# Optimization experiments

Measured on AMD Instinct MI355X. Metric: run time of the kernel, lower is better.

## Reference

```python
import jax, jax.numpy as jnp
import numpy as np

ALPHA = 0.2  # LeakyReLU negative slope

def setup_inputs() -> dict:
    key = jax.random.key(0)
    k1, k2, k3 = jax.random.split(key, 3)
    B, N, Fin, Fout = 8, 2048, 256, 128
    h = jax.random.normal(k1, (B, N, Fin), dtype=jnp.float32)
    W = jax.random.normal(k2, (Fin, Fout), dtype=jnp.float32) * (1.414 / np.sqrt(Fin))
    a = jax.random.normal(k3, (2 * Fout, 1), dtype=jnp.float32) * 0.1
    return {"h": h, "W": W, "a": a}

def reference(h, W, a):
    # Wh: [B, N, D]
    Wh = jnp.einsum('bni,io->bno', h, W)
    D = Wh.shape[-1]
    a1 = a[:D, 0]   # weights for the 'i' (repeat_interleave) half
    a2 = a[D:, 0]   # weights for the 'j' (repeat) half
    s1 = Wh @ a1    # [B, N]
    s2 = Wh @ a2    # [B, N]
    # e[b,i,j] = leakyrelu(s1[b,i] + s2[b,j])  (fused form of the O(N^2*2D) concat)
    e = s1[:, :, None] + s2[:, None, :]
    e = jnp.where(e >= 0, e, ALPHA * e)
    # original applies softmax over dim=1 (the i axis)
    attention = jax.nn.softmax(e, axis=1)
    # dropout is identity in eval mode
    h_prime = jnp.einsum('bij,bjd->bid', attention, Wh)
    # concat=True -> ELU
    return jax.nn.elu(h_prime)
```

## Files before the change

kernel.cpp:

```cpp
#include <hip/hip_runtime.h>
#include <hip/hip_bf16.h>


#define ALPHA 0.2f
#define LOG2E 1.4426950408889634f
constexpr int Bb=8, Nn=2048, FIN=256, FOUT=128;

typedef __attribute__((ext_vector_type(8))) short short8;
typedef __attribute__((ext_vector_type(4))) float f32x4;
typedef __attribute__((ext_vector_type(16))) float f32x16;
typedef const __attribute__((address_space(1))) unsigned int* gptr_t;
typedef __attribute__((address_space(3))) unsigned int* lptr_t;

__device__ __forceinline__ float lrelu(float x){ return fmaxf(x, ALPHA*x); }
__device__ __forceinline__ unsigned short bfbits(float x){
    __hip_bfloat16 h = __float2bfloat16(x);
    return *(unsigned short*)&h;
}

__global__ __launch_bounds__(256) void k_wh(const float* __restrict__ h,
                                            const float* __restrict__ W,
                                            const float* __restrict__ a,
                                            float* __restrict__ s1,
                                            float* __restrict__ s2,
                                            __hip_bfloat16* __restrict__ WhT){
    const int blk = blockIdx.x;
    const int rowbase = blk * 32;
    const int b = blk >> 6;
    const int jt = (rowbase & (Nn-1)) >> 5;
    const int t = threadIdx.x;
    const int wave = t>>6, lane = t&63;
    const int wm = wave & 1, wn = wave >> 1;
    const int lm = lane & 15, q = lane >> 4;

    __shared__ __align__(16) float hs[32*260];
    __shared__ float s1red[2][32], s2red[2][32];

    {
        const float* srcbase = h + (size_t)rowbase*FIN;
        #pragma unroll
        for (int c = 0; c < 8; ++c){
            const int row = wave*8 + c;
            __builtin_amdgcn_global_load_lds(
                (gptr_t)(srcbase + (size_t)row*FIN + lane*4),
                (lptr_t)&hs[row*260], 16, 0, 0);
        }
    }
    __syncthreads();

    f32x4 acc[4];
    #pragma unroll
    for (int ntl = 0; ntl < 4; ++ntl) acc[ntl] = (f32x4){0.f,0.f,0.f,0.f};

    const float* hrow = &hs[(wm*16 + lm)*260];
    const float* Wq   = W + (size_t)(q*8)*FOUT + wn*64 + lm;
    #pragma unroll
    for (int kt = 0; kt < 8; ++kt){
        float av[8];
        *(float4*)&av[0] = *(const float4*)&hrow[kt*32 + q*8];
        *(float4*)&av[4] = *(const float4*)&hrow[kt*32 + q*8 + 4];
        short8 afr;
        #pragma unroll
        for (int e = 0; e < 8; ++e) afr[e] = (short)bfbits(av[e]);
        const float* Wkt = Wq + (size_t)kt*32*FOUT;
        #pragma unroll
        for (int ntl = 0; ntl < 4; ++ntl){
            const float* Wp = Wkt + ntl*16;
            short8 bfr;
            #pragma unroll
            for (int e = 0; e < 8; ++e) bfr[e] = (short)bfbits(Wp[(size_t)e*FOUT]);
            acc[ntl] = __builtin_amdgcn_mfma_f32_16x16x32_bf16(afr, bfr, acc[ntl], 0,0,0);
        }
    }

    {
        float a1v[4], a2v[4];
        #pragma unroll
        for (int ntl = 0; ntl < 4; ++ntl){
            a1v[ntl] = a[wn*64 + ntl*16 + lm];
            a2v[ntl] = a[FOUT + wn*64 + ntl*16 + lm];
        }
        #pragma unroll
        for (int rg = 0; rg < 4; ++rg){
            float p1 = 0.f, p2 = 0.f;
            #pragma unroll
            for (int ntl = 0; ntl < 4; ++ntl){
                p1 += acc[ntl][rg]*a1v[ntl];
                p2 += acc[ntl][rg]*a2v[ntl];
            }
            #pragma unroll
            for (int m = 1; m < 16; m <<= 1){
                p1 += __shfl_xor(p1, m);
                p2 += __shfl_xor(p2, m);
            }
            if (lm == 0){
                s1red[wn][wm*16 + q*4 + rg] = p1;
                s2red[wn][wm*16 + q*4 + rg] = p2;
            }
        }
    }

    {
        short* Wo = (short*)WhT;
        const size_t tb = ((size_t)(b*32 + (jt >> 1)))*8192;
        const int s  = (jt & 1)*2 + wm;
        const int l5 = q >> 1, ehalf = (q & 1)*4;
        #pragma unroll
        for (int ntl = 0; ntl < 4; ++ntl){
            const int d = wn*64 + ntl*16 + lm;
            const int u = (s*4 + (d>>5))*64 + l5*32 + (d & 31);
            ushort4 v;
            v.x = bfbits(acc[ntl][0]); v.y = bfbits(acc[ntl][1]);
            v.z = bfbits(acc[ntl][2]); v.w = bfbits(acc[ntl][3]);
            *(ushort4*)&Wo[tb + (size_t)u*8 + ehalf] = v;
        }
    }

    __syncthreads();
    if (t < 32){
        s1[rowbase + t] = (s1red[0][t] + s1red[1][t]) * LOG2E;
        s2[rowbase + t] = (s2red[0][t] + s2red[1][t]) * LOG2E;
    }
}

__global__ __launch_bounds__(256) void k_z(const float* __restrict__ s1,
                                           const float* __restrict__ s2,
                                           float* __restrict__ Aout,
                                           float* __restrict__ Bout){
    const int b  = blockIdx.x >> 6;
    const int jt = blockIdx.x & 63;
    const int t  = threadIdx.x;
    const int jj = t & 31, part = t >> 5;
    const int j  = jt*32 + jj;
    __shared__ float s1s[Nn];
    __shared__ float red[8][33];

    {
        const float4* g = (const float4*)(s1 + (size_t)b*Nn);
        float4* p = (float4*)s1s;
        #pragma unroll
        for (int v0 = 0; v0 < 2; ++v0){ const int v = t + v0*256; p[v] = g[v]; }
    }
    __syncthreads();
    const float s2j = s2[b*Nn + j];
    float sum = 0.f;
    const float4* s4 = (const float4*)&s1s[part*256];
    #pragma unroll 4
    for (int v = 0; v < 64; ++v){
        float x[4]; *(float4*)x = s4[v];
        sum += __builtin_amdgcn_exp2f(lrelu(x[0]+s2j))
             + __builtin_amdgcn_exp2f(lrelu(x[1]+s2j))
             + __builtin_amdgcn_exp2f(lrelu(x[2]+s2j))
             + __builtin_amdgcn_exp2f(lrelu(x[3]+s2j));
    }
    red[part][jj] = sum;
    __syncthreads();
    if (part == 0){
        float Z = 0.f;
        #pragma unroll
        for (int p = 0; p < 8; ++p) Z += red[p][jj];
        const float lz = -__builtin_amdgcn_logf(Z);
        Aout[b*Nn + j] = s2j + lz;
        Bout[b*Nn + j] = ALPHA*s2j + lz;
    }
}

__global__ __launch_bounds__(512, 2) void k_pv(const float* __restrict__ s1,
                                               const float* __restrict__ Aarr,
                                               const float* __restrict__ Barr,
                                               const __hip_bfloat16* __restrict__ WhT,
                                               float* __restrict__ out){
    const int blk   = blockIdx.x;
    const int b     = blk & 7;
    const int ibase = (blk >> 3) * 64;
    const int t     = threadIdx.x;
    const int wave  = t >> 6, lane = t & 63;
    const int wr = wave & 1, kh = wave >> 1;
    const int il = lane & 31, l5 = lane >> 5;

    __shared__ unsigned short Bs[2][4][8192];

    const float s1a  = s1[(size_t)b*Nn + ibase + wr*32 + il];
    const float as1a = ALPHA * s1a;
    const float* Ab = Aarr + (size_t)b*Nn;
    const float* Zb = Barr + (size_t)b*Nn;

    f32x16 acc[4];
    #pragma unroll
    for (int nt = 0; nt < 4; ++nt)
        #pragma unroll
        for (int e = 0; e < 16; ++e) acc[nt][e] = 0.f;

    const char* Wtb = (const char*)WhT + (size_t)b*32*16384;
    const int laneoff = wr*8192 + lane*16;

    {
        const char* src = Wtb + (size_t)(kh*8)*16384 + laneoff;
        unsigned short* dst = &Bs[0][kh][wr*4096];
        #pragma unroll
        for (int c = 0; c < 8; ++c)
            __builtin_amdgcn_global_load_lds((gptr_t)(src + c*1024),
                                             (lptr_t)(dst + c*512), 16, 0, 0);
    }

    int buf = 0;
    for (int it = 0; it < 8; ++it){
        __syncthreads();
        if (it + 1 < 8){
            const char* src = Wtb + (size_t)(kh*8 + it + 1)*16384 + laneoff;
            unsigned short* dst = &Bs[buf^1][kh][wr*4096];
            #pragma unroll
            for (int c = 0; c < 8; ++c)
                __builtin_amdgcn_global_load_lds((gptr_t)(src + c*1024),
                                                 (lptr_t)(dst + c*512), 16, 0, 0);
        }
        const char* tile = (const char*)&Bs[buf][kh][0];
        #pragma unroll
        for (int s = 0; s < 4; ++s){
            short8 bfr[4];
            #pragma unroll
            for (int nt = 0; nt < 4; ++nt)
                bfr[nt] = *(const short8*)(tile + ((s*4 + nt)*64 + lane)*16);

            const int jb = kh*512 + it*64 + s*16 + l5*8;
            float av[8], bv[8];
            *(float4*)&av[0] = *(const float4*)&Ab[jb];
            *(float4*)&av[4] = *(const float4*)&Ab[jb+4];
            *(float4*)&bv[0] = *(const float4*)&Zb[jb];
            *(float4*)&bv[4] = *(const float4*)&Zb[jb+4];
            short8 afa;
            #pragma unroll
            for (int e = 0; e < 8; ++e)
                afa[e] = (short)bfbits(__builtin_amdgcn_exp2f(
                             fmaxf(s1a + av[e], as1a + bv[e])));
            #pragma unroll
            for (int nt = 0; nt < 4; ++nt)
                acc[nt] = __builtin_amdgcn_mfma_f32_32x32x16_bf16(afa, bfr[nt], acc[nt], 0,0,0);
        }
        buf ^= 1;
    }

    __syncthreads();
    float* comb = (float*)&Bs[0][0][0];
    if (kh < 2){
        float* cb = comb + (size_t)(kh*2 + wr)*(32*132);
        #pragma unroll
        for (int nt = 0; nt < 4; ++nt)
            #pragma unroll
            for (int r = 0; r < 16; ++r){
                const int row = (r&3) + 8*(r>>2) + 4*l5;
                cb[row*132 + nt*32 + il] = acc[nt][r];
            }
    }
    __syncthreads();
    if (kh >= 2){
        float* cb = comb + (size_t)((kh-2)*2 + wr)*(32*132);
        #pragma unroll
        for (int nt = 0; nt < 4; ++nt)
            #pragma unroll
            for (int r = 0; r < 16; ++r){
                const int row = (r&3) + 8*(r>>2) + 4*l5;
                cb[row*132 + nt*32 + il] += acc[nt][r];
            }
    }
    __syncthreads();
    {
        const int rgrp = t >> 5, c4 = (t & 31)*4;
        #pragma unroll
        for (int rr = 0; rr < 4; ++rr){
            const int row = rgrp*4 + rr;
            const int wrr = row >> 5, rin = row & 31;
            const float* r0 = comb + (size_t)(wrr)*(32*132)       + rin*132 + c4;
            const float* r1 = comb + (size_t)(2 + wrr)*(32*132)   + rin*132 + c4;
            float4 v0 = *(const float4*)r0, v1 = *(const float4*)r1;
            float o[4];
            #pragma unroll
            for (int e = 0; e < 4; ++e){
                const float x = ((const float*)&v0)[e] + ((const float*)&v1)[e];
                o[e] = x > 0.f ? x : expm1f(x);
            }
            *(float4*)&out[((size_t)(b*Nn + ibase + row))*FOUT + c4] = *(float4*)o;
        }
    }
}

extern "C" void kernel_launch(void* const* d_in, const int* in_sizes, int n_in,
                              void* d_out, int out_size, void* d_ws, size_t ws_size,
                              hipStream_t stream) {
    (void)in_sizes; (void)n_in; (void)out_size; (void)ws_size;
    const float* h = (const float*)d_in[0];
    const float* W = (const float*)d_in[1];
    const float* a = (const float*)d_in[2];
    float* out = (float*)d_out;

    float* ws    = (float*)d_ws;
    float* s1    = ws;
    float* s2    = s1 + Bb*Nn;
    float* Aarr  = s2 + Bb*Nn;
    float* Barr  = Aarr + Bb*Nn;
    __hip_bfloat16* WhT = (__hip_bfloat16*)(Barr + Bb*Nn);

    k_wh  <<<dim3(Bb*Nn/32),  dim3(256), 0, stream>>>(h, W, a, s1, s2, WhT);
    k_z   <<<dim3(Bb*64),     dim3(256), 0, stream>>>(s1, s2, Aarr, Barr);
    k_pv  <<<dim3(Bb*Nn/64),  dim3(512), 0, stream>>>(s1, Aarr, Barr, WhT, out);
}
```

Before: 105.2 us.

## Replace dense attention matmul with sort-and-prefix-sum separable LeakyReLU formulation

Uses the fact that exp(lrelu(s1_i+s2_j)) splits into exp(s1)exp(s2) or exp(a*s1)exp(a*s2) depending on the sign of s1_i+s2_j. It sorts s1 and s2 per batch, computes softmax normalisers with prefix and suffix sums plus binary search, and computes the output through chunked prefix sums of weighted Wh rows. This turns the O(N^2·D) MFMA attention into roughly O(N log N + N·D) work. In exchange it adds a serial bitonic sort in only 16 blocks, several extra launches, scattered gathers, and possible precision loss from the exp2 of unnormalised scores.

```diff
diff --git a/kernel.cpp b/kernel.cpp
--- a/kernel.cpp
+++ b/kernel.cpp
@@ -5,35 +5,38 @@
 #define ALPHA 0.2f
 #define LOG2E 1.4426950408889634f
 constexpr int Bb=8, Nn=2048, FIN=256, FOUT=128;
+constexpr int NC=32, CH=64;
+constexpr int SUFSTR=2052;
 
 typedef __attribute__((ext_vector_type(8))) short short8;
 typedef __attribute__((ext_vector_type(4))) float f32x4;
-typedef __attribute__((ext_vector_type(16))) float f32x16;
 typedef const __attribute__((address_space(1))) unsigned int* gptr_t;
 typedef __attribute__((address_space(3))) unsigned int* lptr_t;
 
-__device__ __forceinline__ float lrelu(float x){ return fmaxf(x, ALPHA*x); }
 __device__ __forceinline__ unsigned short bfbits(float x){
     __hip_bfloat16 h = __float2bfloat16(x);
     return *(unsigned short*)&h;
 }
+__device__ __forceinline__ float bf2f(unsigned short u){
+    unsigned int w = ((unsigned int)u) << 16;
+    return *(float*)&w;
+}
 
 __global__ __launch_bounds__(256) void k_wh(const float* __restrict__ h,
                                             const float* __restrict__ W,
                                             const float* __restrict__ a,
-                                            float* __restrict__ s1,
-                                            float* __restrict__ s2,
-                                            __hip_bfloat16* __restrict__ WhT){
+                                            float* __restrict__ s1h,
+                                            float* __restrict__ s2h,
+                                            __hip_bfloat16* __restrict__ Whb){
     const int blk = blockIdx.x;
     const int rowbase = blk * 32;
-    const int b = blk >> 6;
-    const int jt = (rowbase & (Nn-1)) >> 5;
     const int t = threadIdx.x;
     const int wave = t>>6, lane = t&63;
     const int wm = wave & 1, wn = wave >> 1;
     const int lm = lane & 15, q = lane >> 4;
 
     __shared__ __align__(16) float hs[32*260];
+    __shared__ __align__(16) float tt2[32][132];
     __shared__ float s1red[2][32], s2red[2][32];
 
     {
@@ -100,186 +103,277 @@
         }
     }
 
-    {
-        short* Wo = (short*)WhT;
-        const size_t tb = ((size_t)(b*32 + (jt >> 1)))*8192;
-        const int s  = (jt & 1)*2 + wm;
-        const int l5 = q >> 1, ehalf = (q & 1)*4;
-        #pragma unroll
-        for (int ntl = 0; ntl < 4; ++ntl){
-            const int d = wn*64 + ntl*16 + lm;
-            const int u = (s*4 + (d>>5))*64 + l5*32 + (d & 31);
-            ushort4 v;
-            v.x = bfbits(acc[ntl][0]); v.y = bfbits(acc[ntl][1]);
-            v.z = bfbits(acc[ntl][2]); v.w = bfbits(acc[ntl][3]);
-            *(ushort4*)&Wo[tb + (size_t)u*8 + ehalf] = v;
-        }
-    }
-
-    __syncthreads();
+    #pragma unroll
+    for (int ntl = 0; ntl < 4; ++ntl)
+        #pragma unroll
+        for (int rg = 0; rg < 4; ++rg)
+            tt2[wm*16 + q*4 + rg][wn*64 + ntl*16 + lm] = acc[ntl][rg];
+    __syncthreads();
+
     if (t < 32){
-        s1[rowbase + t] = (s1red[0][t] + s1red[1][t]) * LOG2E;
-        s2[rowbase + t] = (s2red[0][t] + s2red[1][t]) * LOG2E;
-    }
-}
-
-__global__ __launch_bounds__(256) void k_z(const float* __restrict__ s1,
-                                           const float* __restrict__ s2,
-                                           float* __restrict__ Aout,
-                                           float* __restrict__ Bout){
-    const int b  = blockIdx.x >> 6;
-    const int jt = blockIdx.x & 63;
-    const int t  = threadIdx.x;
-    const int jj = t & 31, part = t >> 5;
-    const int j  = jt*32 + jj;
-    __shared__ float s1s[Nn];
-    __shared__ float red[8][33];
-
-    {
-        const float4* g = (const float4*)(s1 + (size_t)b*Nn);
-        float4* p = (float4*)s1s;
-        #pragma unroll
-        for (int v0 = 0; v0 < 2; ++v0){ const int v = t + v0*256; p[v] = g[v]; }
-    }
-    __syncthreads();
-    const float s2j = s2[b*Nn + j];
-    float sum = 0.f;
-    const float4* s4 = (const float4*)&s1s[part*256];
-    #pragma unroll 4
-    for (int v = 0; v < 64; ++v){
-        float x[4]; *(float4*)x = s4[v];
-        sum += __builtin_amdgcn_exp2f(lrelu(x[0]+s2j))
-             + __builtin_amdgcn_exp2f(lrelu(x[1]+s2j))
-             + __builtin_amdgcn_exp2f(lrelu(x[2]+s2j))
-             + __builtin_amdgcn_exp2f(lrelu(x[3]+s2j));
-    }
-    red[part][jj] = sum;
-    __syncthreads();
-    if (part == 0){
-        float Z = 0.f;
-        #pragma unroll
-        for (int p = 0; p < 8; ++p) Z += red[p][jj];
-        const float lz = -__builtin_amdgcn_logf(Z);
-        Aout[b*Nn + j] = s2j + lz;
-        Bout[b*Nn + j] = ALPHA*s2j + lz;
-    }
-}
-
-__global__ __launch_bounds__(512, 2) void k_pv(const float* __restrict__ s1,
-                                               const float* __restrict__ Aarr,
-                                               const float* __restrict__ Barr,
-                                               const __hip_bfloat16* __restrict__ WhT,
-                                               float* __restrict__ out){
-    const int blk   = blockIdx.x;
-    const int b     = blk & 7;
-    const int ibase = (blk >> 3) * 64;
-    const int t     = threadIdx.x;
-    const int wave  = t >> 6, lane = t & 63;
-    const int wr = wave & 1, kh = wave >> 1;
-    const int il = lane & 31, l5 = lane >> 5;
-
-    __shared__ unsigned short Bs[2][4][8192];
-
-    const float s1a  = s1[(size_t)b*Nn + ibase + wr*32 + il];
-    const float as1a = ALPHA * s1a;
-    const float* Ab = Aarr + (size_t)b*Nn;
-    const float* Zb = Barr + (size_t)b*Nn;
-
-    f32x16 acc[4];
+        s1h[rowbase + t] = (s1red[0][t] + s1red[1][t]) * LOG2E;
+        s2h[rowbase + t] = (s2red[0][t] + s2red[1][t]) * LOG2E;
+    }
+    {
+        const int row = t >> 3, seg = (t & 7) * 16;
+        const float* src = &tt2[row][seg];
+        short8 v0, v1;
+        #pragma unroll
+        for (int e = 0; e < 8; ++e){
+            v0[e] = (short)bfbits(src[e]);
+            v1[e] = (short)bfbits(src[e+8]);
+        }
+        short* dst = (short*)Whb + (size_t)(rowbase + row)*FOUT + seg;
+        *(short8*)dst       = v0;
+        *(short8*)(dst + 8) = v1;
+    }
+}
+
+__global__ __launch_bounds__(1024) void k_sort(const float* __restrict__ s1h,
+                                               const float* __restrict__ s2h,
+                                               float* __restrict__ s1s,
+                                               float* __restrict__ s2s,
+                                               int* __restrict__ ipr,
+                                               int* __restrict__ prm,
+                                               float* __restrict__ SufE,
+                                               float* __restrict__ PreA){
+    const int bb = blockIdx.x;
+    const bool isS1 = bb >= 8;
+    const int b = bb & 7;
+    const int t = threadIdx.x;
+    __shared__ __align__(16) float key[2048];
+    __shared__ __align__(16) int   pay[2048];
+    __shared__ __align__(16) float scb[2048];
+
+    const float* src = (isS1 ? s1h : s2h) + (size_t)b*Nn;
     #pragma unroll
-    for (int nt = 0; nt < 4; ++nt)
-        #pragma unroll
-        for (int e = 0; e < 16; ++e) acc[nt][e] = 0.f;
-
-    const char* Wtb = (const char*)WhT + (size_t)b*32*16384;
-    const int laneoff = wr*8192 + lane*16;
-
-    {
-        const char* src = Wtb + (size_t)(kh*8)*16384 + laneoff;
-        unsigned short* dst = &Bs[0][kh][wr*4096];
-        #pragma unroll
-        for (int c = 0; c < 8; ++c)
-            __builtin_amdgcn_global_load_lds((gptr_t)(src + c*1024),
-                                             (lptr_t)(dst + c*512), 16, 0, 0);
-    }
-
-    int buf = 0;
-    for (int it = 0; it < 8; ++it){
+    for (int v=0; v<2; ++v){ const int i=t+v*1024; key[i]=src[i]; pay[i]=i; }
+    __syncthreads();
+    for (int k=2; k<=2048; k<<=1){
+        for (int j=k>>1; j>0; j>>=1){
+            const int i = ((t & ~(j-1))<<1) | (t & (j-1));
+            const int l = i | j;
+            const bool up = (i & k)==0;
+            const float a0=key[i], a1=key[l];
+            const bool sw = up ? (a0>a1) : (a0<a1);
+            if (sw){
+                key[i]=a1; key[l]=a0;
+                const int p0=pay[i]; pay[i]=pay[l]; pay[l]=p0;
+            }
+            __syncthreads();
+        }
+    }
+    {
+        float* kdst = (isS1 ? s1s : s2s) + (size_t)b*Nn;
+        int*   pdst = (isS1 ? ipr : prm) + (size_t)b*Nn;
+        #pragma unroll
+        for (int v=0; v<2; ++v){ const int i=t+v*1024; kdst[i]=key[i]; pdst[i]=pay[i]; }
+    }
+    if (isS1){
         __syncthreads();
-        if (it + 1 < 8){
-            const char* src = Wtb + (size_t)(kh*8 + it + 1)*16384 + laneoff;
-            unsigned short* dst = &Bs[buf^1][kh][wr*4096];
+        float* bufB = (float*)pay;
+        float* bufC = scb;
+
+        #pragma unroll
+        for (int v=0; v<2; ++v){ const int i=t+v*1024; bufB[i]=__builtin_amdgcn_exp2f(ALPHA*key[i]); }
+        __syncthreads();
+        {
+            float *sp=bufB, *dp=bufC;
+            for (int off=1; off<2048; off<<=1){
+                #pragma unroll
+                for (int v=0; v<2; ++v){
+                    const int i=t+v*1024;
+                    float x = sp[i];
+                    if (i>=off) x += sp[i-off];
+                    dp[i]=x;
+                }
+                __syncthreads();
+                float* tmp=sp; sp=dp; dp=tmp;
+            }
+            float* dst = PreA + (size_t)b*SUFSTR;
             #pragma unroll
-            for (int c = 0; c < 8; ++c)
-                __builtin_amdgcn_global_load_lds((gptr_t)(src + c*1024),
-                                                 (lptr_t)(dst + c*512), 16, 0, 0);
-        }
-        const char* tile = (const char*)&Bs[buf][kh][0];
-        #pragma unroll
-        for (int s = 0; s < 4; ++s){
-            short8 bfr[4];
+            for (int v=0; v<2; ++v){ const int i=t+v*1024; dst[i+1]=sp[i]; }
+            if (t==0) dst[0]=0.f;
+        }
+        __syncthreads();
+        #pragma unroll
+        for (int v=0; v<2; ++v){ const int i=t+v*1024; bufB[i]=__builtin_amdgcn_exp2f(key[i]); }
+        __syncthreads();
+        {
+            float *sp=bufB, *dp=bufC;
+            for (int off=1; off<2048; off<<=1){
+                #pragma unroll
+                for (int v=0; v<2; ++v){
+                    const int i=t+v*1024;
+                    float x = sp[i];
+                    if (i+off<2048) x += sp[i+off];
+                    dp[i]=x;
+                }
+                __syncthreads();
+                float* tmp=sp; sp=dp; dp=tmp;
+            }
+            float* dst = SufE + (size_t)b*SUFSTR;
             #pragma unroll
-            for (int nt = 0; nt < 4; ++nt)
-                bfr[nt] = *(const short8*)(tile + ((s*4 + nt)*64 + lane)*16);
-
-            const int jb = kh*512 + it*64 + s*16 + l5*8;
-            float av[8], bv[8];
-            *(float4*)&av[0] = *(const float4*)&Ab[jb];
-            *(float4*)&av[4] = *(const float4*)&Ab[jb+4];
-            *(float4*)&bv[0] = *(const float4*)&Zb[jb];
-            *(float4*)&bv[4] = *(const float4*)&Zb[jb+4];
-            short8 afa;
-            #pragma unroll
-            for (int e = 0; e < 8; ++e)
-                afa[e] = (short)bfbits(__builtin_amdgcn_exp2f(
-                             fmaxf(s1a + av[e], as1a + bv[e])));
-            #pragma unroll
-            for (int nt = 0; nt < 4; ++nt)
-                acc[nt] = __builtin_amdgcn_mfma_f32_32x32x16_bf16(afa, bfr[nt], acc[nt], 0,0,0);
-        }
-        buf ^= 1;
-    }
-
-    __syncthreads();
-    float* comb = (float*)&Bs[0][0][0];
-    if (kh < 2){
-        float* cb = comb + (size_t)(kh*2 + wr)*(32*132);
-        #pragma unroll
-        for (int nt = 0; nt < 4; ++nt)
-            #pragma unroll
-            for (int r = 0; r < 16; ++r){
-                const int row = (r&3) + 8*(r>>2) + 4*l5;
-                cb[row*132 + nt*32 + il] = acc[nt][r];
-            }
-    }
-    __syncthreads();
-    if (kh >= 2){
-        float* cb = comb + (size_t)((kh-2)*2 + wr)*(32*132);
-        #pragma unroll
-        for (int nt = 0; nt < 4; ++nt)
-            #pragma unroll
-            for (int r = 0; r < 16; ++r){
-                const int row = (r&3) + 8*(r>>2) + 4*l5;
-                cb[row*132 + nt*32 + il] += acc[nt][r];
-            }
-    }
-    __syncthreads();
-    {
-        const int rgrp = t >> 5, c4 = (t & 31)*4;
-        #pragma unroll
-        for (int rr = 0; rr < 4; ++rr){
-            const int row = rgrp*4 + rr;
-            const int wrr = row >> 5, rin = row & 31;
-            const float* r0 = comb + (size_t)(wrr)*(32*132)       + rin*132 + c4;
-            const float* r1 = comb + (size_t)(2 + wrr)*(32*132)   + rin*132 + c4;
-            float4 v0 = *(const float4*)r0, v1 = *(const float4*)r1;
-            float o[4];
-            #pragma unroll
-            for (int e = 0; e < 4; ++e){
-                const float x = ((const float*)&v0)[e] + ((const float*)&v1)[e];
-                o[e] = x > 0.f ? x : expm1f(x);
-            }
-            *(float4*)&out[((size_t)(b*Nn + ibase + row))*FOUT + c4] = *(float4*)o;
+            for (int v=0; v<2; ++v){ const int i=t+v*1024; dst[i]=sp[i]; }
+            if (t==0) dst[2048]=0.f;
+        }
+    }
+}
+
+__global__ __launch_bounds__(256) void k_scanA(const float* __restrict__ s1s,
+                                               const float* __restrict__ s2s,
+                                               const float* __restrict__ SufE,
+                                               const float* __restrict__ PreA,
+                                               const int* __restrict__ prm,
+                                               const __hip_bfloat16* __restrict__ Whb,
+                                               float* __restrict__ c1g,
+                                               float* __restrict__ c2g,
+                                               int* __restrict__ thg,
+                                               float* __restrict__ chS,
+                                               float* __restrict__ chT){
+    const int blk = blockIdx.x;
+    const int b = blk & 7, c = blk >> 3;
+    const int t = threadIdx.x;
+    __shared__ __align__(16) float s1l[2048], s2l[2048];
+    __shared__ __align__(16) float sufl[2052], prel[2052];
+    __shared__ float c1l[CH], c2l[CH];
+    __shared__ int   permc[CH];
+    __shared__ float red[2][2][128];
+
+    {
+        #pragma unroll
+        for (int v=0; v<2; ++v){
+            const int i=t+v*256;
+            ((f32x4*)s1l)[i]  = ((const f32x4*)(s1s  + (size_t)b*Nn))[i];
+            ((f32x4*)s2l)[i]  = ((const f32x4*)(s2s  + (size_t)b*Nn))[i];
+            ((f32x4*)sufl)[i] = ((const f32x4*)(SufE + (size_t)b*SUFSTR))[i];
+            ((f32x4*)prel)[i] = ((const f32x4*)(PreA + (size_t)b*SUFSTR))[i];
+        }
+        if (t==0){
+            sufl[2048] = SufE[(size_t)b*SUFSTR + 2048];
+            prel[2048] = PreA[(size_t)b*SUFSTR + 2048];
+        }
+        if (t<CH) permc[t] = prm[(size_t)b*Nn + c*CH + t];
+    }
+    __syncthreads();
+    if (t < CH){
+        const int q = c*CH + t;
+        const float s2v = s2l[q];
+        int lo=0, hi=Nn;
+        while (lo<hi){ const int mid=(lo+hi)>>1; if (s1l[mid] < -s2v) lo=mid+1; else hi=mid; }
+        const float e1 = __builtin_amdgcn_exp2f(s2v);
+        const float ea = __builtin_amdgcn_exp2f(ALPHA*s2v);
+        const float Z  = e1*sufl[lo] + ea*prel[lo];
+        const float iz = 1.f/Z;
+        c1l[t] = e1*iz;  c2l[t] = ea*iz;
+        c1g[(size_t)b*Nn + q] = c1l[t];
+        c2g[(size_t)b*Nn + q] = c2l[t];
+        const float s1v = s1l[q];
+        int lo2=0, hi2=Nn;
+        while (lo2<hi2){ const int mid=(lo2+hi2)>>1; if (s2l[mid] < -s1v) lo2=mid+1; else hi2=mid; }
+        thg[(size_t)b*Nn + q] = lo2;
+    }
+    __syncthreads();
+    {
+        const int qh = t>>7, d = t&127;
+        float sA=0.f, sB=0.f;
+        #pragma unroll 8
+        for (int qq=0; qq<32; ++qq){
+            const int ql = qh*32 + qq;
+            const float w = bf2f(((const unsigned short*)Whb)[((size_t)b*Nn + permc[ql])*FOUT + d]);
+            sA += c1l[ql]*w;
+            sB += c2l[ql]*w;
+        }
+        red[0][qh][d]=sA; red[1][qh][d]=sB;
+    }
+    __syncthreads();
+    if (t < 128)      chS[((size_t)b*NC + c)*128 + t]       = red[0][0][t] + red[0][1][t];
+    else { const int d=t-128; chT[((size_t)b*NC + c)*128 + d] = red[1][0][d] + red[1][1][d]; }
+}
+
+__global__ __launch_bounds__(256) void k_scanOut(const float* __restrict__ s1s,
+                                                 const int* __restrict__ ipr,
+                                                 const int* __restrict__ prm,
+                                                 const int* __restrict__ thg,
+                                                 const float* __restrict__ c1g,
+                                                 const float* __restrict__ c2g,
+                                                 const float* __restrict__ chS,
+                                                 const float* __restrict__ chT,
+                                                 const __hip_bfloat16* __restrict__ Whb,
+                                                 float* __restrict__ out){
+    const int blk = blockIdx.x;
+    const int b = blk & 7, c = blk >> 3;
+    const int t = threadIdx.x;
+    __shared__ __align__(16) float s1l[2048];
+    __shared__ __align__(16) int   thl[2048];
+    __shared__ __align__(16) int   iprl[2048];
+    __shared__ int   permc[CH];
+    __shared__ float c1l[CH], c2l[CH];
+    __shared__ __align__(16) float whl[CH][128];
+    __shared__ __align__(16) float Sloc[CH+1][128], Tloc[CH+1][128];
+
+    {
+        #pragma unroll
+        for (int v=0; v<2; ++v){
+            const int i=t+v*256;
+            ((f32x4*)s1l)[i] = ((const f32x4*)(s1s + (size_t)b*Nn))[i];
+            ((int4*)thl)[i]  = ((const int4*)(thg + (size_t)b*Nn))[i];
+            ((int4*)iprl)[i] = ((const int4*)(ipr + (size_t)b*Nn))[i];
+        }
+        if (t<CH){
+            permc[t] = prm[(size_t)b*Nn + c*CH + t];
+            c1l[t]   = c1g[(size_t)b*Nn + c*CH + t];
+            c2l[t]   = c2g[(size_t)b*Nn + c*CH + t];
+        }
+    }
+    __syncthreads();
+    {
+        for (int v=0; v<32; ++v){
+            const int e = v*256 + t;
+            const int row = e>>7, d = e&127;
+            whl[row][d] = bf2f(((const unsigned short*)Whb)[((size_t)b*Nn + permc[row])*FOUT + d]);
+        }
+    }
+    float sc=0.f, tc=0.f;
+    if (t < 128){
+        #pragma unroll
+        for (int cc=0; cc<NC; ++cc){
+            if (cc > c) sc += chS[((size_t)b*NC + cc)*128 + t];
+            if (cc < c) tc += chT[((size_t)b*NC + cc)*128 + t];
+        }
+    }
+    __syncthreads();
+    if (t < 128){
+        const int d = t;
+        float run = sc;
+        Sloc[CH][d] = run;
+        #pragma unroll 8
+        for (int p=CH-1; p>=0; --p){ run += c1l[p]*whl[p][d]; Sloc[p][d]=run; }
+        float run2 = tc;
+        Tloc[0][d] = run2;
+        #pragma unroll 8
+        for (int p=0; p<CH; ++p){ run2 += c2l[p]*whl[p][d]; Tloc[p+1][d]=run2; }
+    }
+    __syncthreads();
+    const int U = (c==NC-1) ? (Nn+1) : (c*CH + CH);
+    const int L = c*CH;
+    int lo=0, hi=Nn;
+    while (lo<hi){ const int mid=(lo+hi)>>1; if (thl[mid] < U) hi=mid; else lo=mid+1; }
+    const int r_lo = lo;
+    lo=0; hi=Nn;
+    while (lo<hi){ const int mid=(lo+hi)>>1; if (thl[mid] < L) hi=mid; else lo=mid+1; }
+    const int r_hi = lo;
+
+    const int half = t>>7, d = t&127;
+    for (int rr=r_lo; rr<r_hi; rr+=2){
+        const int r = rr + half;
+        if (r < r_hi){
+            const int p = thl[r] - L;
+            const float s1v = s1l[r];
+            const float u1 = __builtin_amdgcn_exp2f(s1v);
+            const float u2 = __builtin_amdgcn_exp2f(ALPHA*s1v);
+            const float x = u1*Sloc[p][d] + u2*Tloc[p][d];
+            out[((size_t)b*Nn + iprl[r])*FOUT + d] = x > 0.f ? x : expm1f(x);
         }
     }
 }
@@ -293,14 +387,26 @@
     const float* a = (const float*)d_in[2];
     float* out = (float*)d_out;
 
-    float* ws    = (float*)d_ws;
-    float* s1    = ws;
-    float* s2    = s1 + Bb*Nn;
-    float* Aarr  = s2 + Bb*Nn;
-    float* Barr  = Aarr + Bb*Nn;
-    __hip_bfloat16* WhT = (__hip_bfloat16*)(Barr + Bb*Nn);
-
-    k_wh  <<<dim3(Bb*Nn/32),  dim3(256), 0, stream>>>(h, W, a, s1, s2, WhT);
-    k_z   <<<dim3(Bb*64),     dim3(256), 0, stream>>>(s1, s2, Aarr, Barr);
-    k_pv  <<<dim3(Bb*Nn/64),  dim3(512), 0, stream>>>(s1, Aarr, Barr, WhT, out);
-}
+    float* ws   = (float*)d_ws;
+    float* s1h  = ws;
+    float* s2h  = s1h + Bb*Nn;
+    float* s1s  = s2h + Bb*Nn;
+    float* s2s  = s1s + Bb*Nn;
+    float* SufE = s2s + Bb*Nn;
+    float* PreA = SufE + Bb*SUFSTR;
+    float* c1g  = PreA + Bb*SUFSTR;
+    float* c2g  = c1g + Bb*Nn;
+    float* chS  = c2g + Bb*Nn;
+    float* chT  = chS + Bb*NC*128;
+    int*   thg  = (int*)(chT + Bb*NC*128);
+    int*   prm  = thg + Bb*Nn;
+    int*   ipr  = prm + Bb*Nn;
+    __hip_bfloat16* Whb = (__hip_bfloat16*)(ipr + Bb*Nn);
+
+    k_wh     <<<dim3(Bb*Nn/32), dim3(256),  0, stream>>>(h, W, a, s1h, s2h, Whb);
+    k_sort   <<<dim3(16),       dim3(1024), 0, stream>>>(s1h, s2h, s1s, s2s, ipr, prm, SufE, PreA);
+    k_scanA  <<<dim3(Bb*NC),    dim3(256),  0, stream>>>(s1s, s2s, SufE, PreA, prm, Whb,
+                                                         c1g, c2g, thg, chS, chT);
+    k_scanOut<<<dim3(Bb*NC),    dim3(256),  0, stream>>>(s1s, ipr, prm, thg, c1g, c2g,
+                                                         chS, chT, Whb, out);
+}
```

After: 129.6 us. 23.2% more time.
